# Kernel optimization log

Hardware: AMD Instinct MI355X
Metric: run time of the kernel (lower is better)

Reference implementation:

```python
import jax, jax.numpy as jnp
import numpy as np

BN_EPS = 1e-3  # Keras BatchNormalization default epsilon


def _conv_block(x, k):
    """Per-task conv (stride 2, pad 1) -> ReLU -> BatchNorm (center/scale=False, training).

    x: [B, E, H, W, Cin]  (B tasks, E examples per task)
    k: [B, kh, kw, Cin, Cout]  per-task kernel
    """
    def conv_one(xe, kt):  # xe: [E,H,W,Cin], kt: [kh,kw,Cin,Cout]
        return jax.lax.conv_general_dilated(
            xe, kt, window_strides=(2, 2), padding=[(1, 1), (1, 1)],
            dimension_numbers=('NHWC', 'HWIO', 'NHWC'))
    y = jax.nn.relu(jax.vmap(conv_one)(x, k))  # [B,E,H',W',Cout]
    # BatchNorm in training mode: moments over all axes except channels
    m = jnp.mean(y, axis=(0, 1, 2, 3))
    v = jnp.var(y, axis=(0, 1, 2, 3))
    return (y - m) * jax.lax.rsqrt(v + BN_EPS)


def setup_inputs() -> dict:
    key = jax.random.key(0)
    ks = jax.random.split(key, 6)
    B, E, H, C, O = 64, 64, 28, 64, 20
    return {
        'x': jax.random.normal(ks[0], (B, E, H, H, 1), dtype=jnp.float32),
        'k1': jax.random.normal(ks[1], (B, 3, 3, 1, C), dtype=jnp.float32) * 0.1,
        'k2': jax.random.normal(ks[2], (B, 3, 3, C, C), dtype=jnp.float32) * 0.05,
        'k3': jax.random.normal(ks[3], (B, 3, 3, C, C), dtype=jnp.float32) * 0.05,
        'k4': jax.random.normal(ks[4], (B, 3, 3, C, C), dtype=jnp.float32) * 0.05,
        'w_ro': jax.random.normal(ks[5], (B, C, O), dtype=jnp.float32) * 0.1,
    }


def reference(x, k1, k2, k3, k4, w_ro):
    h = _conv_block(x, k1)   # [B,E,14,14,C]
    h = _conv_block(h, k2)   # [B,E,7,7,C]
    h = _conv_block(h, k3)   # [B,E,4,4,C]
    h = _conv_block(h, k4)   # [B,E,2,2,C]
    # MaxPooling2D with pool size == full spatial extent -> global spatial max
    feat = jnp.max(h, axis=(2, 3))  # [B,E,C]
    # per-task readout matmul: [B,E,H] x [B,H,O] -> [B,E,O]
    return jnp.einsum('beh,bho->beo', feat, w_ro)
```

## Files before the change

### kernel.cpp

```cpp
#include <hip/hip_runtime.h>

#define BN_EPS 1e-3f

typedef __attribute__((ext_vector_type(8))) short bf16x8;
typedef __attribute__((ext_vector_type(16))) float floatx16;
typedef unsigned short u16;

__device__ __forceinline__ u16 f2bf(float f) {
  unsigned u = __float_as_uint(f);
  u += 0x7fffu + ((u >> 16) & 1u);
  return (u16)(u >> 16);
}
__device__ __forceinline__ float bf2f(u16 h) {
  return __uint_as_float(((unsigned)h) << 16);
}

static constexpr int NSHARD = 256;

__global__ __launch_bounds__(256) void conv1_kernel(
    const float* __restrict__ x, const float* __restrict__ k1,
    u16* __restrict__ y1, float* __restrict__ statsSh)
{
  __shared__ float xp[900];
  __shared__ float w1[576];
  __shared__ float red[256];

  const int be = blockIdx.x, b = be >> 6, tid = threadIdx.x;

  for (int i = tid; i < 900; i += 256) xp[i] = 0.f;
  for (int i = tid; i < 576; i += 256) w1[i] = k1[(size_t)b * 576 + i];
  __syncthreads();
  for (int i = tid; i < 784; i += 256) {
    const int r = i / 28, cc = i - 28 * r;
    xp[(r + 1) * 30 + (cc + 1)] = x[(size_t)be * 784 + i];
  }
  __syncthreads();

  const int c = tid & 63;
  float wr[9];
#pragma unroll
  for (int t = 0; t < 9; ++t) wr[t] = w1[t * 64 + c];

  float sum = 0.f, ss = 0.f;
  for (int pix = tid >> 6; pix < 196; pix += 4) {
    const int oy = pix / 14, ox = pix - 14 * oy;
    const float* xb = &xp[(2 * oy) * 30 + 2 * ox];
    float acc = 0.f;
#pragma unroll
    for (int ky = 0; ky < 3; ++ky)
#pragma unroll
      for (int kx = 0; kx < 3; ++kx)
        acc = fmaf(xb[ky * 30 + kx], wr[ky * 3 + kx], acc);
    const float v = fmaxf(acc, 0.f);
    y1[((size_t)be * 196 + pix) * 64 + c] = f2bf(v);
    sum += v;
    ss = fmaf(v, v, ss);
  }

  red[tid] = sum;
  __syncthreads();
  if (tid < 64)
    atomicAdd(&statsSh[(blockIdx.x & (NSHARD - 1)) * 128 + tid],
              red[tid] + red[tid + 64] + red[tid + 128] + red[tid + 192]);
  __syncthreads();
  red[tid] = ss;
  __syncthreads();
  if (tid < 64)
    atomicAdd(&statsSh[(blockIdx.x & (NSHARD - 1)) * 128 + 64 + tid],
              red[tid] + red[tid + 64] + red[tid + 128] + red[tid + 192]);
}

__global__ __launch_bounds__(256) void fold_kernel(
    const float* __restrict__ W, const float* __restrict__ statsSh, float invN,
    u16* __restrict__ Wf, float* __restrict__ biasCls)
{
  __shared__ float T[64 * 68];
  __shared__ float P[256];
  __shared__ float s1[64], t1[64];
  __shared__ float tbS[64];

  const int b = blockIdx.x / 3, sg = blockIdx.x % 3;
  const int tid = threadIdx.x;

  {
    const int g = tid >> 7, cidx = tid & 127;
    float acc = 0.f;
    for (int k = 0; k < 128; ++k) acc += statsSh[(g * 128 + k) * 128 + cidx];
    P[tid] = acc;
  }
  __syncthreads();
  if (tid < 64) {
    const float m = (P[tid] + P[tid + 128]) * invN;
    const float var = fmaf(-m, m, (P[64 + tid] + P[192 + tid]) * invN);
    const float s = rsqrtf(var + BN_EPS);
    s1[tid] = s;
    t1[tid] = -m * s;
  }
  __syncthreads();

  const int cin = tid >> 2, q0 = (tid & 3) * 16;
  const int cout = tid >> 2, ci0 = (tid & 3) * 16;
  for (int s = sg * 3; s < sg * 3 + 3; ++s) {
    if (tid < 64) tbS[tid] = 0.f;
    const float* ss = W + ((size_t)b * 9 + s) * 4096;
#pragma unroll
    for (int q = 0; q < 16; q += 4) {
      const float4 v = *(const float4*)(ss + cin * 64 + q0 + q);
      T[(q0 + q + 0) * 68 + cin] = v.x;
      T[(q0 + q + 1) * 68 + cin] = v.y;
      T[(q0 + q + 2) * 68 + cin] = v.z;
      T[(q0 + q + 3) * 68 + cin] = v.w;
    }
    __syncthreads();
    alignas(16) u16 tmp[16];
    float tb = 0.f;
#pragma unroll
    for (int j = 0; j < 16; ++j) {
      const float wv = T[cout * 68 + ci0 + j];
      tmp[j] = f2bf(wv * s1[ci0 + j]);
      tb = fmaf(t1[ci0 + j], wv, tb);
    }
    u16* dst = Wf + ((size_t)b * 9 + s) * 4096 + cout * 64 + ci0;
    *(uint4*)dst       = *(uint4*)&tmp[0];
    *(uint4*)(dst + 8) = *(uint4*)&tmp[8];
    atomicAdd(&tbS[cout], tb);
    __syncthreads();
    if (tid < 64) {
      const int ky = s / 3, kx = s % 3;
      const float tv = tbS[tid];
#pragma unroll
      for (int cls = 0; cls < 9; ++cls) {
        const int ry = cls / 3, rx = cls % 3;
        const bool valid = !((ry == 1 && ky == 0) || (ry == 2 && ky == 2) ||
                             (rx == 1 && kx == 0) || (rx == 2 && kx == 2));
        if (valid) atomicAdd(&biasCls[(size_t)b * 576 + cls * 64 + tid], tv);
      }
    }
    __syncthreads();
  }
}

template <int Hin, int Hout, int G>
__global__ __launch_bounds__(256) void conv_gemm_kernel(
    const u16* __restrict__ yin, const u16* __restrict__ Wf,
    const float* __restrict__ biasCls, u16* __restrict__ yout,
    float* __restrict__ statsSh)
{
  constexpr int PPI  = Hout * Hout;
  constexpr int ROWS = G * PPI;
  constexpr int BPT  = 64 / G;

  __shared__ __align__(16) u16 AS[256 * 72];
  __shared__ __align__(16) u16 BtS[64 * 72];
  __shared__ float biasS[576];
  __shared__ float redsum[64], redss[64];

  const int b = blockIdx.x / BPT;
  const int e0 = (blockIdx.x % BPT) * G;
  const int tid = threadIdx.x, lane = tid & 63, wave = tid >> 6;

  for (int i = tid; i < 576; i += 256) biasS[i] = biasCls[(size_t)b * 576 + i];
  if (tid < 64) { redsum[tid] = 0.f; redss[tid] = 0.f; }

  const int row = tid;
  const bool rowOk = row < ROWS;
  const int g = rowOk ? row / PPI : 0;
  const int pp = rowOk ? row % PPI : 0;
  const int oy = pp / Hout, ox = pp % Hout;
  const size_t inBase = ((size_t)(b * 64 + e0 + g)) * (Hin * Hin) * 64;

  if (!rowOk) {
#pragma unroll
    for (int j = 0; j < 8; ++j) *(uint4*)&AS[row * 72 + j * 8] = uint4{0, 0, 0, 0};
  }

  const int bco = tid >> 2, bci = (tid & 3) * 16;

  const int m0 = wave * 64;
  const int l31 = lane & 31;
  const int kq = (lane >> 5) * 8;

  floatx16 acc00, acc01, acc10, acc11;
#pragma unroll
  for (int r = 0; r < 16; ++r) { acc00[r] = 0.f; acc01[r] = 0.f; acc10[r] = 0.f; acc11[r] = 0.f; }

#pragma unroll
  for (int s = 0; s < 9; ++s) {
    const int ky = s / 3, kx = s % 3;
    if (rowOk) {
      const int iy = 2 * oy - 1 + ky, ix = 2 * ox - 1 + kx;
      const bool ok = ((unsigned)iy < (unsigned)Hin) && ((unsigned)ix < (unsigned)Hin);
      if (ok) {
        const u16* src = yin + inBase + (size_t)(iy * Hin + ix) * 64;
#pragma unroll
        for (int j = 0; j < 8; ++j)
          *(uint4*)&AS[row * 72 + j * 8] = *(const uint4*)(src + j * 8);
      } else {
#pragma unroll
        for (int j = 0; j < 8; ++j) *(uint4*)&AS[row * 72 + j * 8] = uint4{0, 0, 0, 0};
      }
    }
    {
      const u16* gw = Wf + ((size_t)b * 9 + s) * 4096 + bco * 64 + bci;
      *(uint4*)&BtS[bco * 72 + bci]     = *(const uint4*)gw;
      *(uint4*)&BtS[bco * 72 + bci + 8] = *(const uint4*)(gw + 8);
    }
    __syncthreads();
#pragma unroll
    for (int kk = 0; kk < 4; ++kk) {
      const int ko = kk * 16 + kq;
      bf16x8 a0 = *(const bf16x8*)&AS[(m0 + l31) * 72 + ko];
      bf16x8 a1 = *(const bf16x8*)&AS[(m0 + 32 + l31) * 72 + ko];
      bf16x8 b0 = *(const bf16x8*)&BtS[l31 * 72 + ko];
      bf16x8 b1 = *(const bf16x8*)&BtS[(32 + l31) * 72 + ko];
      acc00 = __builtin_amdgcn_mfma_f32_32x32x16_bf16(a0, b0, acc00, 0, 0, 0);
      acc01 = __builtin_amdgcn_mfma_f32_32x32x16_bf16(a0, b1, acc01, 0, 0, 0);
      acc10 = __builtin_amdgcn_mfma_f32_32x32x16_bf16(a1, b0, acc10, 0, 0, 0);
      acc11 = __builtin_amdgcn_mfma_f32_32x32x16_bf16(a1, b1, acc11, 0, 0, 0);
    }
    __syncthreads();
  }

  float ls0 = 0.f, lss0 = 0.f, ls1 = 0.f, lss1 = 0.f;
  const int col0 = l31, col1 = 32 + l31;
  const int rb = m0 + 4 * (lane >> 5);
#pragma unroll
  for (int mt = 0; mt < 2; ++mt) {
    const floatx16& aN0 = mt ? acc10 : acc00;
    const floatx16& aN1 = mt ? acc11 : acc01;
#pragma unroll
    for (int r = 0; r < 16; ++r) {
      const int rw = rb + mt * 32 + (r & 3) + 8 * (r >> 2);
      if (rw < ROWS) {
        const int re = rw / PPI, pr = rw % PPI;
        const int ooy = pr / Hout, oox = pr % Hout;
        const int ry = (ooy == 0) ? 1 : ((2 * ooy + 1 >= Hin) ? 2 : 0);
        const int rx = (oox == 0) ? 1 : ((2 * oox + 1 >= Hin) ? 2 : 0);
        const int cls = ry * 3 + rx;
        const size_t ob = ((size_t)(b * 64 + e0 + re) * PPI + pr) * 64;
        const float v0 = fmaxf(aN0[r] + biasS[cls * 64 + col0], 0.f);
        const float v1 = fmaxf(aN1[r] + biasS[cls * 64 + col1], 0.f);
        yout[ob + col0] = f2bf(v0);
        yout[ob + col1] = f2bf(v1);
        ls0 += v0; lss0 = fmaf(v0, v0, lss0);
        ls1 += v1; lss1 = fmaf(v1, v1, lss1);
      }
    }
  }
  atomicAdd(&redsum[col0], ls0);
  atomicAdd(&redss[col0], lss0);
  atomicAdd(&redsum[col1], ls1);
  atomicAdd(&redss[col1], lss1);
  __syncthreads();
  if (tid < 64) {
    const int sh = blockIdx.x & (NSHARD - 1);
    atomicAdd(&statsSh[sh * 128 + tid], redsum[tid]);
    atomicAdd(&statsSh[sh * 128 + 64 + tid], redss[tid]);
  }
}

__global__ __launch_bounds__(256) void readout_kernel(
    const u16* __restrict__ y4, const float* __restrict__ w_ro,
    const float* __restrict__ statsSh, float invN, float* __restrict__ outp)
{
  __shared__ float wl[64 * 20];
  __shared__ float feat[64 * 64];
  __shared__ float P[256];
  __shared__ float sArr[64], tArr[64];

  const int b = blockIdx.x, tid = threadIdx.x;

  {
    const int g = tid >> 7, cidx = tid & 127;
    float acc = 0.f;
    for (int k = 0; k < 128; ++k) acc += statsSh[(g * 128 + k) * 128 + cidx];
    P[tid] = acc;
  }
  for (int i = tid; i < 1280; i += 256) wl[i] = w_ro[(size_t)b * 1280 + i];
  __syncthreads();
  if (tid < 64) {
    const float m = (P[tid] + P[tid + 128]) * invN;
    const float var = fmaf(-m, m, (P[64 + tid] + P[192 + tid]) * invN);
    const float s = rsqrtf(var + BN_EPS);
    sArr[tid] = s;
    tArr[tid] = -m * s;
  }
  __syncthreads();

  {
    const int e = tid & 63;
    for (int c = tid >> 6; c < 64; c += 4) {
      const u16* p4 = y4 + ((size_t)(b * 64 + e) * 4) * 64 + c;
      const float v = fmaxf(fmaxf(bf2f(p4[0]), bf2f(p4[64])),
                            fmaxf(bf2f(p4[128]), bf2f(p4[192])));
      feat[c * 64 + e] = fmaf(v, sArr[c], tArr[c]);
    }
  }
  __syncthreads();

  const int e = tid >> 2, og = (tid & 3) * 5;
  float acc[5] = {0.f, 0.f, 0.f, 0.f, 0.f};
  for (int c = 0; c < 64; ++c) {
    const float f = feat[c * 64 + e];
#pragma unroll
    for (int j = 0; j < 5; ++j) acc[j] = fmaf(f, wl[c * 20 + og + j], acc[j]);
  }
#pragma unroll
  for (int j = 0; j < 5; ++j)
    outp[((size_t)b * 64 + e) * 20 + og + j] = acc[j];
}

extern "C" void kernel_launch(void* const* d_in, const int* in_sizes, int n_in,
                              void* d_out, int out_size, void* d_ws, size_t ws_size,
                              hipStream_t stream) {
  (void)in_sizes; (void)n_in; (void)out_size; (void)ws_size;
  const float* x   = (const float*)d_in[0];
  const float* k1  = (const float*)d_in[1];
  const float* k2  = (const float*)d_in[2];
  const float* k3  = (const float*)d_in[3];
  const float* k4  = (const float*)d_in[4];
  const float* wro = (const float*)d_in[5];
  float* out = (float*)d_out;
  char* ws = (char*)d_ws;

  float* stats = (float*)ws;
  float* bias2 = (float*)(ws + 524288);
  float* bias3 = bias2 + 36864;
  float* bias4 = bias3 + 36864;
  u16* k2f = (u16*)(ws + 524288 + 442368);
  u16* k3f = k2f + (size_t)2359296;
  u16* k4f = k3f + (size_t)2359296;
  u16* y2 = k4f + (size_t)2359296;
  u16* y1 = y2 + (size_t)12845056;
  u16* y3 = y1;
  u16* y4 = y3 + (size_t)4194304;

  float* st1 = stats;
  float* st2 = stats + 32768;
  float* st3 = stats + 65536;
  float* st4 = stats + 98304;

  hipMemsetAsync(stats, 0, 524288 + 442368, stream);

  conv1_kernel<<<4096, 256, 0, stream>>>(x, k1, y1, st1);
  fold_kernel<<<192, 256, 0, stream>>>(k2, st1, 1.f / 802816.f, k2f, bias2);
  conv_gemm_kernel<14, 7, 4><<<1024, 256, 0, stream>>>(y1, k2f, bias2, y2, st2);
  fold_kernel<<<192, 256, 0, stream>>>(k3, st2, 1.f / 200704.f, k3f, bias3);
  conv_gemm_kernel<7, 4, 16><<<256, 256, 0, stream>>>(y2, k3f, bias3, y3, st3);
  fold_kernel<<<192, 256, 0, stream>>>(k4, st3, 1.f / 65536.f, k4f, bias4);
  conv_gemm_kernel<4, 2, 64><<<64, 256, 0, stream>>>(y3, k4f, bias4, y4, st4);
  readout_kernel<<<64, 256, 0, stream>>>(y4, wro, st4, 1.f / 16384.f, out);
}
```

Baseline: 270.4 us.

## Halve conv GEMM tile, prefetch next slice into registers, shrink stats shards

The conv GEMM kernel now handles 128 output rows per block instead of 256, doubling the grid for each layer, and each wave computes one 32-row M tile with two MFMA accumulators. The global loads for the next kernel-tap slice are issued into registers before the current MFMA loop runs, so loading overlaps with compute. LDS row padding shrinks from 72 to 68. Stats shards drop from 256 to 64, which means less memset and fewer reduction reads but more atomic contention per shard.

```diff
diff --git a/kernel.cpp b/kernel.cpp
--- a/kernel.cpp
+++ b/kernel.cpp
@@ -15,7 +15,7 @@
   return __uint_as_float(((unsigned)h) << 16);
 }
 
-static constexpr int NSHARD = 256;
+static constexpr int NSHARD = 64;
 
 __global__ __launch_bounds__(256) void conv1_kernel(
     const float* __restrict__ x, const float* __restrict__ k1,
@@ -85,7 +85,8 @@
   {
     const int g = tid >> 7, cidx = tid & 127;
     float acc = 0.f;
-    for (int k = 0; k < 128; ++k) acc += statsSh[(g * 128 + k) * 128 + cidx];
+    for (int k = 0; k < NSHARD / 2; ++k)
+      acc += statsSh[(g * (NSHARD / 2) + k) * 128 + cidx];
     P[tid] = acc;
   }
   __syncthreads();
@@ -149,9 +150,10 @@
   constexpr int PPI  = Hout * Hout;
   constexpr int ROWS = G * PPI;
   constexpr int BPT  = 64 / G;
-
-  __shared__ __align__(16) u16 AS[256 * 72];
-  __shared__ __align__(16) u16 BtS[64 * 72];
+  constexpr int LDA  = 68;
+
+  __shared__ __align__(16) u16 AS[128 * LDA];
+  __shared__ __align__(16) u16 BtS[64 * LDA];
   __shared__ float biasS[576];
   __shared__ float redsum[64], redss[64];
 
@@ -162,61 +164,61 @@
   for (int i = tid; i < 576; i += 256) biasS[i] = biasCls[(size_t)b * 576 + i];
   if (tid < 64) { redsum[tid] = 0.f; redss[tid] = 0.f; }
 
-  const int row = tid;
-  const bool rowOk = row < ROWS;
-  const int g = rowOk ? row / PPI : 0;
-  const int pp = rowOk ? row % PPI : 0;
+  const int arow = tid >> 1, ci0 = (tid & 1) * 32;
+  const bool rowOk = arow < ROWS;
+  const int g = rowOk ? arow / PPI : 0;
+  const int pp = rowOk ? arow % PPI : 0;
   const int oy = pp / Hout, ox = pp % Hout;
   const size_t inBase = ((size_t)(b * 64 + e0 + g)) * (Hin * Hin) * 64;
 
-  if (!rowOk) {
-#pragma unroll
-    for (int j = 0; j < 8; ++j) *(uint4*)&AS[row * 72 + j * 8] = uint4{0, 0, 0, 0};
-  }
-
   const int bco = tid >> 2, bci = (tid & 3) * 16;
-
-  const int m0 = wave * 64;
+  const u16* wbase = Wf + (size_t)b * 9 * 4096 + bco * 64 + bci;
+
+  uint4 pa0, pa1, pa2, pa3, pb0, pb1;
+  auto loadSlice = [&](int s) {
+    const int ky = s / 3, kx = s % 3;
+    const int iy = 2 * oy - 1 + ky, ix = 2 * ox - 1 + kx;
+    if (rowOk && (unsigned)iy < (unsigned)Hin && (unsigned)ix < (unsigned)Hin) {
+      const u16* src = yin + inBase + (size_t)(iy * Hin + ix) * 64 + ci0;
+      pa0 = *(const uint4*)(src);
+      pa1 = *(const uint4*)(src + 8);
+      pa2 = *(const uint4*)(src + 16);
+      pa3 = *(const uint4*)(src + 24);
+    } else {
+      pa0 = pa1 = pa2 = pa3 = uint4{0, 0, 0, 0};
+    }
+    const u16* wsl = wbase + s * 4096;
+    pb0 = *(const uint4*)wsl;
+    pb1 = *(const uint4*)(wsl + 8);
+  };
+
+  const int m0 = wave * 32;
   const int l31 = lane & 31;
   const int kq = (lane >> 5) * 8;
 
-  floatx16 acc00, acc01, acc10, acc11;
-#pragma unroll
-  for (int r = 0; r < 16; ++r) { acc00[r] = 0.f; acc01[r] = 0.f; acc10[r] = 0.f; acc11[r] = 0.f; }
-
+  floatx16 acc0, acc1;
+#pragma unroll
+  for (int r = 0; r < 16; ++r) { acc0[r] = 0.f; acc1[r] = 0.f; }
+
+  loadSlice(0);
 #pragma unroll
   for (int s = 0; s < 9; ++s) {
-    const int ky = s / 3, kx = s % 3;
-    if (rowOk) {
-      const int iy = 2 * oy - 1 + ky, ix = 2 * ox - 1 + kx;
-      const bool ok = ((unsigned)iy < (unsigned)Hin) && ((unsigned)ix < (unsigned)Hin);
-      if (ok) {
-        const u16* src = yin + inBase + (size_t)(iy * Hin + ix) * 64;
-#pragma unroll
-        for (int j = 0; j < 8; ++j)
-          *(uint4*)&AS[row * 72 + j * 8] = *(const uint4*)(src + j * 8);
-      } else {
-#pragma unroll
-        for (int j = 0; j < 8; ++j) *(uint4*)&AS[row * 72 + j * 8] = uint4{0, 0, 0, 0};
-      }
-    }
-    {
-      const u16* gw = Wf + ((size_t)b * 9 + s) * 4096 + bco * 64 + bci;
-      *(uint4*)&BtS[bco * 72 + bci]     = *(const uint4*)gw;
-      *(uint4*)&BtS[bco * 72 + bci + 8] = *(const uint4*)(gw + 8);
-    }
-    __syncthreads();
+    *(uint4*)&AS[arow * LDA + ci0]      = pa0;
+    *(uint4*)&AS[arow * LDA + ci0 + 8]  = pa1;
+    *(uint4*)&AS[arow * LDA + ci0 + 16] = pa2;
+    *(uint4*)&AS[arow * LDA + ci0 + 24] = pa3;
+    *(uint4*)&BtS[bco * LDA + bci]     = pb0;
+    *(uint4*)&BtS[bco * LDA + bci + 8] = pb1;
+    __syncthreads();
+    if (s < 8) loadSlice(s + 1);
 #pragma unroll
     for (int kk = 0; kk < 4; ++kk) {
       const int ko = kk * 16 + kq;
-      bf16x8 a0 = *(const bf16x8*)&AS[(m0 + l31) * 72 + ko];
-      bf16x8 a1 = *(const bf16x8*)&AS[(m0 + 32 + l31) * 72 + ko];
-      bf16x8 b0 = *(const bf16x8*)&BtS[l31 * 72 + ko];
-      bf16x8 b1 = *(const bf16x8*)&BtS[(32 + l31) * 72 + ko];
-      acc00 = __builtin_amdgcn_mfma_f32_32x32x16_bf16(a0, b0, acc00, 0, 0, 0);
-      acc01 = __builtin_amdgcn_mfma_f32_32x32x16_bf16(a0, b1, acc01, 0, 0, 0);
-      acc10 = __builtin_amdgcn_mfma_f32_32x32x16_bf16(a1, b0, acc10, 0, 0, 0);
-      acc11 = __builtin_amdgcn_mfma_f32_32x32x16_bf16(a1, b1, acc11, 0, 0, 0);
+      bf16x8 a  = *(const bf16x8*)&AS[(m0 + l31) * LDA + ko];
+      bf16x8 b0 = *(const bf16x8*)&BtS[l31 * LDA + ko];
+      bf16x8 b1 = *(const bf16x8*)&BtS[(32 + l31) * LDA + ko];
+      acc0 = __builtin_amdgcn_mfma_f32_32x32x16_bf16(a, b0, acc0, 0, 0, 0);
+      acc1 = __builtin_amdgcn_mfma_f32_32x32x16_bf16(a, b1, acc1, 0, 0, 0);
     }
     __syncthreads();
   }
@@ -225,26 +227,21 @@
   const int col0 = l31, col1 = 32 + l31;
   const int rb = m0 + 4 * (lane >> 5);
 #pragma unroll
-  for (int mt = 0; mt < 2; ++mt) {
-    const floatx16& aN0 = mt ? acc10 : acc00;
-    const floatx16& aN1 = mt ? acc11 : acc01;
-#pragma unroll
-    for (int r = 0; r < 16; ++r) {
-      const int rw = rb + mt * 32 + (r & 3) + 8 * (r >> 2);
-      if (rw < ROWS) {
-        const int re = rw / PPI, pr = rw % PPI;
-        const int ooy = pr / Hout, oox = pr % Hout;
-        const int ry = (ooy == 0) ? 1 : ((2 * ooy + 1 >= Hin) ? 2 : 0);
-        const int rx = (oox == 0) ? 1 : ((2 * oox + 1 >= Hin) ? 2 : 0);
-        const int cls = ry * 3 + rx;
-        const size_t ob = ((size_t)(b * 64 + e0 + re) * PPI + pr) * 64;
-        const float v0 = fmaxf(aN0[r] + biasS[cls * 64 + col0], 0.f);
-        const float v1 = fmaxf(aN1[r] + biasS[cls * 64 + col1], 0.f);
-        yout[ob + col0] = f2bf(v0);
-        yout[ob + col1] = f2bf(v1);
-        ls0 += v0; lss0 = fmaf(v0, v0, lss0);
-        ls1 += v1; lss1 = fmaf(v1, v1, lss1);
-      }
+  for (int r = 0; r < 16; ++r) {
+    const int rw = rb + (r & 3) + 8 * (r >> 2);
+    if (rw < ROWS) {
+      const int re = rw / PPI, pr = rw % PPI;
+      const int ooy = pr / Hout, oox = pr % Hout;
+      const int ry = (ooy == 0) ? 1 : ((2 * ooy + 1 >= Hin) ? 2 : 0);
+      const int rx = (oox == 0) ? 1 : ((2 * oox + 1 >= Hin) ? 2 : 0);
+      const int cls = ry * 3 + rx;
+      const size_t ob = ((size_t)(b * 64 + e0 + re) * PPI + pr) * 64;
+      const float v0 = fmaxf(acc0[r] + biasS[cls * 64 + col0], 0.f);
+      const float v1 = fmaxf(acc1[r] + biasS[cls * 64 + col1], 0.f);
+      yout[ob + col0] = f2bf(v0);
+      yout[ob + col1] = f2bf(v1);
+      ls0 += v0; lss0 = fmaf(v0, v0, lss0);
+      ls1 += v1; lss1 = fmaf(v1, v1, lss1);
     }
   }
   atomicAdd(&redsum[col0], ls0);
@@ -273,7 +270,8 @@
   {
     const int g = tid >> 7, cidx = tid & 127;
     float acc = 0.f;
-    for (int k = 0; k < 128; ++k) acc += statsSh[(g * 128 + k) * 128 + cidx];
+    for (int k = 0; k < NSHARD / 2; ++k)
+      acc += statsSh[(g * (NSHARD / 2) + k) * 128 + cidx];
     P[tid] = acc;
   }
   for (int i = tid; i < 1280; i += 256) wl[i] = w_ro[(size_t)b * 1280 + i];
@@ -324,10 +322,10 @@
   char* ws = (char*)d_ws;
 
   float* stats = (float*)ws;
-  float* bias2 = (float*)(ws + 524288);
+  float* bias2 = (float*)(ws + 131072);
   float* bias3 = bias2 + 36864;
   float* bias4 = bias3 + 36864;
-  u16* k2f = (u16*)(ws + 524288 + 442368);
+  u16* k2f = (u16*)(ws + 131072 + 442368);
   u16* k3f = k2f + (size_t)2359296;
   u16* k4f = k3f + (size_t)2359296;
   u16* y2 = k4f + (size_t)2359296;
@@ -336,18 +334,18 @@
   u16* y4 = y3 + (size_t)4194304;
 
   float* st1 = stats;
-  float* st2 = stats + 32768;
-  float* st3 = stats + 65536;
-  float* st4 = stats + 98304;
-
-  hipMemsetAsync(stats, 0, 524288 + 442368, stream);
+  float* st2 = stats + 8192;
+  float* st3 = stats + 16384;
+  float* st4 = stats + 24576;
+
+  hipMemsetAsync(stats, 0, 131072 + 442368, stream);
 
   conv1_kernel<<<4096, 256, 0, stream>>>(x, k1, y1, st1);
   fold_kernel<<<192, 256, 0, stream>>>(k2, st1, 1.f / 802816.f, k2f, bias2);
-  conv_gemm_kernel<14, 7, 4><<<1024, 256, 0, stream>>>(y1, k2f, bias2, y2, st2);
+  conv_gemm_kernel<14, 7, 2><<<2048, 256, 0, stream>>>(y1, k2f, bias2, y2, st2);
   fold_kernel<<<192, 256, 0, stream>>>(k3, st2, 1.f / 200704.f, k3f, bias3);
-  conv_gemm_kernel<7, 4, 16><<<256, 256, 0, stream>>>(y2, k3f, bias3, y3, st3);
+  conv_gemm_kernel<7, 4, 8><<<512, 256, 0, stream>>>(y2, k3f, bias3, y3, st3);
   fold_kernel<<<192, 256, 0, stream>>>(k4, st3, 1.f / 65536.f, k4f, bias4);
-  conv_gemm_kernel<4, 2, 64><<<64, 256, 0, stream>>>(y3, k4f, bias4, y4, st4);
+  conv_gemm_kernel<4, 2, 32><<<128, 256, 0, stream>>>(y3, k4f, bias4, y4, st4);
   readout_kernel<<<64, 256, 0, stream>>>(y4, wro, st4, 1.f / 16384.f, out);
 }
```

Result: slower. 309.9 us (+14.6%).
